# Kernel optimization log

Hardware: AMD Instinct MI355X
Metric: run time of the kernel (lower is better)

## Reference

```python
import jax, jax.numpy as jnp
import numpy as np

VOCAB = 67
EMB = 32
BRANCH = 32
OUT = 96
L = 16
B = 131072


def setup_inputs() -> dict:
    key = jax.random.key(0)
    ks = jax.random.split(key, 10)
    x = jax.random.randint(ks[0], (B, L), 0, VOCAB, dtype=jnp.int64)
    embed = jax.random.normal(ks[1], (VOCAB, EMB), dtype=jnp.float32) * 0.1
    w2 = jax.random.normal(ks[2], (BRANCH, EMB, 2), dtype=jnp.float32) * 0.1
    b2 = jnp.zeros((BRANCH,), jnp.float32)
    w3 = jax.random.normal(ks[3], (BRANCH, EMB, 3), dtype=jnp.float32) * 0.1
    b3 = jnp.zeros((BRANCH,), jnp.float32)
    w4 = jax.random.normal(ks[4], (BRANCH, EMB, 4), dtype=jnp.float32) * 0.1
    b4 = jnp.zeros((BRANCH,), jnp.float32)
    pw = jax.random.normal(ks[5], (OUT, 3 * BRANCH), dtype=jnp.float32) * 0.02
    pb = jnp.zeros((OUT,), jnp.float32)
    return {"x": x, "embed": embed, "w2": w2, "b2": b2, "w3": w3,
            "b3": b3, "w4": w4, "b4": b4, "pw": pw, "pb": pb}


def _branch(emb_ncl, w, b):
    # emb_ncl: [B, EMB, L]; w: [BRANCH, EMB, k] -> conv valid, ReLU, max over time
    y = jax.lax.conv_general_dilated(
        emb_ncl, w, window_strides=(1,), padding='VALID',
        dimension_numbers=('NCH', 'OIH', 'NCH'))
    y = jax.nn.relu(y + b[None, :, None])
    return jnp.max(y, axis=2)  # [B, BRANCH]


def reference(x, embed, w2, b2, w3, b3, w4, b4, pw, pb):
    # padding_idx=0: row 0 of the table is zeros
    table = embed.at[0].set(0.0)
    emb = table[x]                      # [B, L, EMB]
    emb = jnp.transpose(emb, (0, 2, 1))  # [B, EMB, L]
    g2 = _branch(emb, w2, b2)
    g3 = _branch(emb, w3, b3)
    g4 = _branch(emb, w4, b4)
    feat = jnp.concatenate([g2, g3, g4], axis=1)  # [B, 96]
    # Linear + ReLU (dropout is identity at eval)
    return jax.nn.relu(feat @ pw.T + pb)
```

## Files before the change

### kernel.cpp

```cpp
#include <hip/hip_runtime.h>
#include <hip/hip_fp16.h>


#define VOCABSZ 67
#define EMBSZ   32
#define NCH     32
#define NFEAT   96
#define SEQL    16
#define BATCH   131072
#define NTAB    9
#define NENT    (NTAB * VOCABSZ)
#define TABU    (NENT * NCH / 2)
#define PWOFF   TABU
#define NFP     (NFEAT / 2)
#define NPW     (NFEAT * NFP)
#define ESTR    80
#define LTS     (VOCABSZ * ESTR)
#define LDSB    (NTAB * LTS)

typedef _Float16 v2h __attribute__((ext_vector_type(2)));
typedef _Float16 v8h __attribute__((ext_vector_type(8)));
typedef float    v4f __attribute__((ext_vector_type(4)));

__device__ __forceinline__ unsigned packh2(float a, float b) {
    v2h p; p[0] = (_Float16)a; p[1] = (_Float16)b;
    return __builtin_bit_cast(unsigned, p);
}

__global__ __launch_bounds__(256) void build_tables(
    const float* __restrict__ embed,
    const float* __restrict__ w2, const float* __restrict__ b2,
    const float* __restrict__ w3, const float* __restrict__ b3,
    const float* __restrict__ w4, const float* __restrict__ b4,
    const float* __restrict__ pw,
    unsigned* __restrict__ ws)
{
    int idx = blockIdx.x * 256 + threadIdx.x;
    if (idx < TABU) {
        int cp = idx & 15;
        int t  = idx >> 4;
        int j  = t / VOCABSZ;
        int v  = t - j * VOCABSZ;
        const float* w; const float* bias; int k, h;
        if (j < 2)      { w = w2; k = 2; h = j;     bias = (h == 0) ? b2 : nullptr; }
        else if (j < 5) { w = w3; k = 3; h = j - 2; bias = (h == 0) ? b3 : nullptr; }
        else            { w = w4; k = 4; h = j - 5; bias = (h == 0) ? b4 : nullptr; }
        int c0 = 2 * cp;
        float a0 = bias ? bias[c0]     : 0.0f;
        float a1 = bias ? bias[c0 + 1] : 0.0f;
        if (v != 0) {
            #pragma unroll
            for (int e = 0; e < EMBSZ; ++e) {
                float ev = embed[v * EMBSZ + e];
                a0 += ev * w[((c0    ) * EMBSZ + e) * k + h];
                a1 += ev * w[((c0 + 1) * EMBSZ + e) * k + h];
            }
        }
        ws[t * 16 + cp] = packh2(a0, a1);
    } else if (idx < TABU + NPW) {
        int i  = idx - TABU;
        int o  = i / NFP;
        int fp = i - o * NFP;
        ws[PWOFF + i] = packh2(pw[o * NFEAT + 2 * fp], pw[o * NFEAT + 2 * fp + 1]);
    }
}

template<int K, int N, int P0, int TB>
__device__ __forceinline__ void lconv(const char* __restrict__ base,
                                      const int (&ap)[16], v8h& m)
{
    v8h s[N];
    #pragma unroll
    for (int u = 0; u < N; ++u)
        s[u] = *reinterpret_cast<const v8h*>(base + TB + ap[P0 + u]);
    #pragma unroll
    for (int h = 1; h < K; ++h) {
        v8h t[N];
        #pragma unroll
        for (int u = 0; u < N; ++u)
            t[u] = *reinterpret_cast<const v8h*>(base + TB + h * LTS + ap[P0 + u + h]);
        #pragma unroll
        for (int u = 0; u < N; ++u) s[u] = s[u] + t[u];
    }
    #pragma unroll
    for (int u = 0; u < N; ++u) m = __builtin_elementwise_max(m, s[u]);
}

__global__ __launch_bounds__(512, 6) void fused_cnn(
    const int*      __restrict__ x,
    const unsigned* __restrict__ ws,
    const float*    __restrict__ pb,
    float*          __restrict__ out)
{
    extern __shared__ __align__(16) char ldsraw[];
    const int tid = threadIdx.x;
    {
        const float4* s4 = reinterpret_cast<const float4*>(ws);
        float4* d4 = reinterpret_cast<float4*>(ldsraw);
        #pragma unroll
        for (int i0 = 0; i0 < 2560; i0 += 512) {
            int i = i0 + tid;
            if (i < 2412) {
                int t = i >> 2, c = i & 3;
                d4[5 * t + c] = s4[i];
            }
        }
    }
    __syncthreads();

    const int lane = tid & 63;
    const int wv   = tid >> 6;
    const int ml   = lane & 15;
    const int c    = lane >> 4;
    const int co   = c << 4;
    const int rowb = blockIdx.x * 128 + wv * 16;
    const int row  = rowb + ml;
    const char* base = ldsraw;

    const int4* xp = reinterpret_cast<const int4*>(x + row * SEQL);
    int4 q0 = xp[0], q1 = xp[1], q2 = xp[2], q3 = xp[3];
    int ap[16];
    ap[ 0] = q0.x * ESTR + co; ap[ 1] = q0.y * ESTR + co;
    ap[ 2] = q0.z * ESTR + co; ap[ 3] = q0.w * ESTR + co;
    ap[ 4] = q1.x * ESTR + co; ap[ 5] = q1.y * ESTR + co;
    ap[ 6] = q1.z * ESTR + co; ap[ 7] = q1.w * ESTR + co;
    ap[ 8] = q2.x * ESTR + co; ap[ 9] = q2.y * ESTR + co;
    ap[10] = q2.z * ESTR + co; ap[11] = q2.w * ESTR + co;
    ap[12] = q3.x * ESTR + co; ap[13] = q3.y * ESTR + co;
    ap[14] = q3.z * ESTR + co; ap[15] = q3.w * ESTR + co;

    v8h m2 = {}, m3 = {}, m4 = {};

    lconv<2, 5,  0, 0 * LTS>(base, ap, m2);
    lconv<2, 5,  5, 0 * LTS>(base, ap, m2);
    lconv<2, 5, 10, 0 * LTS>(base, ap, m2);
    lconv<3, 5,  0, 2 * LTS>(base, ap, m3);
    lconv<3, 5,  5, 2 * LTS>(base, ap, m3);
    lconv<3, 4, 10, 2 * LTS>(base, ap, m3);
    lconv<4, 5,  0, 5 * LTS>(base, ap, m4);
    lconv<4, 4,  5, 5 * LTS>(base, ap, m4);
    lconv<4, 4,  9, 5 * LTS>(base, ap, m4);

    const unsigned* __restrict__ pwp = ws + PWOFF + ml * NFP + c * 4;
    #pragma unroll
    for (int u = 0; u < 6; ++u) {
        v4f acc = {0.f, 0.f, 0.f, 0.f};
        v8h b0 = *reinterpret_cast<const v8h*>(pwp + 768 * u);
        v8h b1 = *reinterpret_cast<const v8h*>(pwp + 768 * u + 16);
        v8h b2 = *reinterpret_cast<const v8h*>(pwp + 768 * u + 32);
        acc = __builtin_amdgcn_mfma_f32_16x16x32_f16(m2, b0, acc, 0, 0, 0);
        acc = __builtin_amdgcn_mfma_f32_16x16x32_f16(m3, b1, acc, 0, 0, 0);
        acc = __builtin_amdgcn_mfma_f32_16x16x32_f16(m4, b2, acc, 0, 0, 0);
        float pbl = pb[16 * u + ml];
        #pragma unroll
        for (int r = 0; r < 4; ++r)
            out[(size_t)(rowb + c * 4 + r) * NFEAT + 16 * u + ml] =
                fmaxf(acc[r] + pbl, 0.f);
    }
}

extern "C" void kernel_launch(void* const* d_in, const int* in_sizes, int n_in,
                              void* d_out, int out_size, void* d_ws, size_t ws_size,
                              hipStream_t stream)
{
    const int*   x     = (const int*)  d_in[0];
    const float* embed = (const float*)d_in[1];
    const float* w2    = (const float*)d_in[2];
    const float* b2    = (const float*)d_in[3];
    const float* w3    = (const float*)d_in[4];
    const float* b3    = (const float*)d_in[5];
    const float* w4    = (const float*)d_in[6];
    const float* b4    = (const float*)d_in[7];
    const float* pw    = (const float*)d_in[8];
    const float* pb    = (const float*)d_in[9];
    float* out = (float*)d_out;
    unsigned* ws = (unsigned*)d_ws;

    build_tables<<<(TABU + NPW + 255) / 256, 256, 0, stream>>>(
        embed, w2, b2, w3, b3, w4, b4, pw, ws);

    (void)hipFuncSetAttribute((const void*)fused_cnn,
                              hipFuncAttributeMaxDynamicSharedMemorySize,
                              LDSB);
    fused_cnn<<<BATCH / 128, 512, LDSB, stream>>>(x, ws, pb, out);
}
```

Before: 41.00 us.

## Use persistent blocks with atomic work-stealing over row chunks

Launches a fixed set of 768 persistent blocks instead of one block per 128-row chunk. Each block fills its LDS tables once, then repeatedly claims chunks through a global atomic counter that build_tables zeroes. This amortises the per-block LDS table fill across several chunks. It adds an atomic and two block barriers per chunk, and it relies on 768 resident blocks being a good fit for the device.

```diff
diff --git a/kernel.cpp b/kernel.cpp
--- a/kernel.cpp
+++ b/kernel.cpp
@@ -9,14 +9,15 @@
 #define SEQL    16
 #define BATCH   131072
 #define NTAB    9
-#define NENT    (NTAB * VOCABSZ)
-#define TABU    (NENT * NCH / 2)
-#define PWOFF   TABU
 #define NFP     (NFEAT / 2)
-#define NPW     (NFEAT * NFP)
+#define TABU    9648
+#define PWOFF   9648
+#define NPW     4608
+#define CNTW    14336
+#define NCHUNK  1024
 #define ESTR    80
 #define LTS     (VOCABSZ * ESTR)
-#define LDSB    (NTAB * LTS)
+#define LDSB    (NTAB * LTS + 16)
 
 typedef _Float16 v2h __attribute__((ext_vector_type(2)));
 typedef _Float16 v8h __attribute__((ext_vector_type(8)));
@@ -36,6 +37,7 @@
     unsigned* __restrict__ ws)
 {
     int idx = blockIdx.x * 256 + threadIdx.x;
+    if (idx == CNTW) ws[idx] = 0u;
     if (idx < TABU) {
         int cp = idx & 15;
         int t  = idx >> 4;
@@ -58,7 +60,7 @@
         }
         ws[t * 16 + cp] = packh2(a0, a1);
     } else if (idx < TABU + NPW) {
-        int i  = idx - TABU;
+        int i  = idx - PWOFF;
         int o  = i / NFP;
         int fp = i - o * NFP;
         ws[PWOFF + i] = packh2(pw[o * NFEAT + 2 * fp], pw[o * NFEAT + 2 * fp + 1]);
@@ -88,7 +90,7 @@
 
 __global__ __launch_bounds__(512, 6) void fused_cnn(
     const int*      __restrict__ x,
-    const unsigned* __restrict__ ws,
+    unsigned*       __restrict__ ws,
     const float*    __restrict__ pb,
     float*          __restrict__ out)
 {
@@ -101,61 +103,70 @@
         for (int i0 = 0; i0 < 2560; i0 += 512) {
             int i = i0 + tid;
             if (i < 2412) {
-                int t = i >> 2, c = i & 3;
-                d4[5 * t + c] = s4[i];
+                int t = i >> 2, cc = i & 3;
+                d4[5 * t + cc] = s4[i];
             }
         }
     }
-    __syncthreads();
+    volatile int* slot = reinterpret_cast<volatile int*>(ldsraw + NTAB * LTS);
+    unsigned* cnt = ws + CNTW;
 
     const int lane = tid & 63;
     const int wv   = tid >> 6;
     const int ml   = lane & 15;
     const int c    = lane >> 4;
     const int co   = c << 4;
-    const int rowb = blockIdx.x * 128 + wv * 16;
-    const int row  = rowb + ml;
     const char* base = ldsraw;
+    const unsigned* __restrict__ pwp = ws + PWOFF + ml * NFP + c * 4;
 
-    const int4* xp = reinterpret_cast<const int4*>(x + row * SEQL);
-    int4 q0 = xp[0], q1 = xp[1], q2 = xp[2], q3 = xp[3];
-    int ap[16];
-    ap[ 0] = q0.x * ESTR + co; ap[ 1] = q0.y * ESTR + co;
-    ap[ 2] = q0.z * ESTR + co; ap[ 3] = q0.w * ESTR + co;
-    ap[ 4] = q1.x * ESTR + co; ap[ 5] = q1.y * ESTR + co;
-    ap[ 6] = q1.z * ESTR + co; ap[ 7] = q1.w * ESTR + co;
-    ap[ 8] = q2.x * ESTR + co; ap[ 9] = q2.y * ESTR + co;
-    ap[10] = q2.z * ESTR + co; ap[11] = q2.w * ESTR + co;
-    ap[12] = q3.x * ESTR + co; ap[13] = q3.y * ESTR + co;
-    ap[14] = q3.z * ESTR + co; ap[15] = q3.w * ESTR + co;
+    for (;;) {
+        if (tid == 0) *slot = (int)atomicAdd(cnt, 1u);
+        __syncthreads();
+        const int chunk = *slot;
+        __syncthreads();
+        if (chunk >= NCHUNK) break;
 
-    v8h m2 = {}, m3 = {}, m4 = {};
+        const int rowb = chunk * 128 + wv * 16;
+        const int row  = rowb + ml;
 
-    lconv<2, 5,  0, 0 * LTS>(base, ap, m2);
-    lconv<2, 5,  5, 0 * LTS>(base, ap, m2);
-    lconv<2, 5, 10, 0 * LTS>(base, ap, m2);
-    lconv<3, 5,  0, 2 * LTS>(base, ap, m3);
-    lconv<3, 5,  5, 2 * LTS>(base, ap, m3);
-    lconv<3, 4, 10, 2 * LTS>(base, ap, m3);
-    lconv<4, 5,  0, 5 * LTS>(base, ap, m4);
-    lconv<4, 4,  5, 5 * LTS>(base, ap, m4);
-    lconv<4, 4,  9, 5 * LTS>(base, ap, m4);
+        const int4* xp = reinterpret_cast<const int4*>(x + row * SEQL);
+        int4 q0 = xp[0], q1 = xp[1], q2 = xp[2], q3 = xp[3];
+        int ap[16];
+        ap[ 0] = q0.x * ESTR + co; ap[ 1] = q0.y * ESTR + co;
+        ap[ 2] = q0.z * ESTR + co; ap[ 3] = q0.w * ESTR + co;
+        ap[ 4] = q1.x * ESTR + co; ap[ 5] = q1.y * ESTR + co;
+        ap[ 6] = q1.z * ESTR + co; ap[ 7] = q1.w * ESTR + co;
+        ap[ 8] = q2.x * ESTR + co; ap[ 9] = q2.y * ESTR + co;
+        ap[10] = q2.z * ESTR + co; ap[11] = q2.w * ESTR + co;
+        ap[12] = q3.x * ESTR + co; ap[13] = q3.y * ESTR + co;
+        ap[14] = q3.z * ESTR + co; ap[15] = q3.w * ESTR + co;
 
-    const unsigned* __restrict__ pwp = ws + PWOFF + ml * NFP + c * 4;
-    #pragma unroll
-    for (int u = 0; u < 6; ++u) {
-        v4f acc = {0.f, 0.f, 0.f, 0.f};
-        v8h b0 = *reinterpret_cast<const v8h*>(pwp + 768 * u);
-        v8h b1 = *reinterpret_cast<const v8h*>(pwp + 768 * u + 16);
-        v8h b2 = *reinterpret_cast<const v8h*>(pwp + 768 * u + 32);
-        acc = __builtin_amdgcn_mfma_f32_16x16x32_f16(m2, b0, acc, 0, 0, 0);
-        acc = __builtin_amdgcn_mfma_f32_16x16x32_f16(m3, b1, acc, 0, 0, 0);
-        acc = __builtin_amdgcn_mfma_f32_16x16x32_f16(m4, b2, acc, 0, 0, 0);
-        float pbl = pb[16 * u + ml];
+        v8h m2 = {}, m3 = {}, m4 = {};
+        lconv<2, 5,  0, 0 * LTS>(base, ap, m2);
+        lconv<2, 5,  5, 0 * LTS>(base, ap, m2);
+        lconv<2, 5, 10, 0 * LTS>(base, ap, m2);
+        lconv<3, 5,  0, 2 * LTS>(base, ap, m3);
+        lconv<3, 5,  5, 2 * LTS>(base, ap, m3);
+        lconv<3, 4, 10, 2 * LTS>(base, ap, m3);
+        lconv<4, 5,  0, 5 * LTS>(base, ap, m4);
+        lconv<4, 4,  5, 5 * LTS>(base, ap, m4);
+        lconv<4, 4,  9, 5 * LTS>(base, ap, m4);
+
         #pragma unroll
-        for (int r = 0; r < 4; ++r)
-            out[(size_t)(rowb + c * 4 + r) * NFEAT + 16 * u + ml] =
-                fmaxf(acc[r] + pbl, 0.f);
+        for (int u = 0; u < 6; ++u) {
+            v4f acc = {0.f, 0.f, 0.f, 0.f};
+            v8h w0 = *reinterpret_cast<const v8h*>(pwp + 768 * u);
+            v8h w1 = *reinterpret_cast<const v8h*>(pwp + 768 * u + 16);
+            v8h w2 = *reinterpret_cast<const v8h*>(pwp + 768 * u + 32);
+            acc = __builtin_amdgcn_mfma_f32_16x16x32_f16(m2, w0, acc, 0, 0, 0);
+            acc = __builtin_amdgcn_mfma_f32_16x16x32_f16(m3, w1, acc, 0, 0, 0);
+            acc = __builtin_amdgcn_mfma_f32_16x16x32_f16(m4, w2, acc, 0, 0, 0);
+            float pbl = pb[16 * u + ml];
+            #pragma unroll
+            for (int r = 0; r < 4; ++r)
+                out[(size_t)(rowb + c * 4 + r) * NFEAT + 16 * u + ml] =
+                    fmaxf(acc[r] + pbl, 0.f);
+        }
     }
 }
 
@@ -176,11 +187,11 @@
     float* out = (float*)d_out;
     unsigned* ws = (unsigned*)d_ws;
 
-    build_tables<<<(TABU + NPW + 255) / 256, 256, 0, stream>>>(
+    build_tables<<<(CNTW + 256) / 256, 256, 0, stream>>>(
         embed, w2, b2, w3, b3, w4, b4, pw, ws);
 
     (void)hipFuncSetAttribute((const void*)fused_cnn,
                               hipFuncAttributeMaxDynamicSharedMemorySize,
                               LDSB);
-    fused_cnn<<<BATCH / 128, 512, LDSB, stream>>>(x, ws, pb, out);
+    fused_cnn<<<768, 512, LDSB, stream>>>(x, ws, pb, out);
 }
```

Result: slower. 49.45 us (+20.6%).
